# Kernel tuning notes

Measured on AMD Instinct MI355X. Metric: run time of the kernel, lower is better.

Reference implementation:

```python
import jax, jax.numpy as jnp
import numpy as np

N = 70
NT = 2485
M_DIM = 2000
SQ2 = float(np.sqrt(2.0))
SQH = float(np.sqrt(0.5))
_r, _c = np.tril_indices(N)
ROWS = jnp.asarray(_r)
COLS = jnp.asarray(_c)


def smat(x):
    # svec^{-1}: lower-tri fill (row-major) then symmetrize with sqrt(2) off-diag scaling
    v = jnp.reshape(x, (-1,))
    L = jnp.zeros((N, N), v.dtype).at[ROWS, COLS].set(v)
    return SQH * (L + L.T) - (SQ2 - 1.0) * L * jnp.eye(N, dtype=v.dtype)


def svec(X):
    Y = SQ2 * X - (SQ2 - 1.0) * X * jnp.eye(N, dtype=X.dtype)
    return Y[ROWS, COLS].reshape(NT, 1)


def skmult(G, K, Amat):
    # vectorized version of the per-column loop: for each column a of Amat,
    # 0.5 * svec(K smat(a) G^T + G smat(a) K^T)
    S = jax.vmap(smat, in_axes=1)(Amat)                      # [L, N, N]
    T = jnp.einsum('ij,ljk,hk->lih', K, S, G) + jnp.einsum('ij,ljk,hk->lih', G, S, K)
    return jax.vmap(svec)(0.5 * T)[:, :, 0].T                # [NT, L]


def Hp_op(U, P, Pinv):
    return 0.5 * (P @ U @ Pinv + Pinv.T @ U.T @ P.T)


def _steplen(d, Rinv, gcur):
    lam0 = jnp.linalg.eigvalsh(Rinv.T @ smat(d) @ Rinv)[0]   # smallest eigenvalue
    s = jnp.where(lam0 < 0, -1.0 / lam0, 20.0)
    return jnp.minimum(0.5, gcur * s)


def setup_inputs() -> dict:
    key = jax.random.key(0)
    ks = jax.random.split(key, 6)
    R1 = jax.random.normal(ks[0], (N, N), jnp.float32)
    X0 = R1 @ R1.T + N * jnp.eye(N, dtype=jnp.float32)
    R2 = jax.random.normal(ks[1], (N, N), jnp.float32)
    Z0 = R2 @ R2.T + N * jnp.eye(N, dtype=jnp.float32)
    x = svec(X0)
    z = svec(Z0)
    A = jax.random.normal(ks[2], (M_DIM, NT), jnp.float32) / np.float32(np.sqrt(NT))
    y = jax.random.normal(ks[3], (M_DIM, 1), jnp.float32)
    b = A @ x + 0.1 * jax.random.normal(ks[4], (M_DIM, 1), jnp.float32)
    c = z + A.T @ y + 0.1 * jax.random.normal(ks[5], (NT, 1), jnp.float32)
    normc = jnp.full((1, 1), 3.7, jnp.float32)
    return {'x': x, 'y': y, 'z': z, 'A': A, 'b': b, 'c': c, 'normc': normc}


def reference(x, y, z, A, b, c, normc):
    tol = 1e-6
    X = smat(x)
    Z = smat(z)
    Q = jnp.linalg.cholesky(X).T        # upper factor: X = Q^T Q
    P = jnp.linalg.cholesky(Z).T
    Qinv = jnp.linalg.inv(Q)
    Pinv = jnp.linalg.inv(P)
    Zinv = jnp.linalg.inv(Z)
    rp = b - A @ x
    Rd = c - z - A.T @ y
    mu = (x[:, 0] @ z[:, 0]) / 70.0
    # predictor
    Rc = -svec(Hp_op(X @ Z, P, Pinv))
    Mmat = A @ skmult(X, Zinv, A.T)
    Minv = jnp.linalg.inv(Mmat)
    h = rp + A @ (skmult(X, Zinv, Rd) - skmult(Pinv, Pinv, Rc))
    dy = Minv @ h
    dz = Rd - A.T @ dy
    dx = -x - skmult(X, Zinv, dz)
    alpha = _steplen(dx, Qinv, 0.9)
    beta = _steplen(dz, Pinv, 0.9)
    minab = jnp.minimum(alpha, beta)
    e = jnp.where((mu > tol) & (minab >= jnp.sqrt(1.0 / 3.0)),
                  jnp.maximum(1.0, 3.0 * minab * minab), 1.0)
    dot_new = (x + alpha * dx)[:, 0] @ (z + beta * dz)[:, 0]
    frac = dot_new / (x[:, 0] @ z[:, 0])
    frac_safe = jnp.where(dot_new < 0, 1.0, frac)
    sigma = jnp.where(dot_new < 0, 0.8, jnp.minimum(1.0, frac_safe ** e))
    # corrector
    Rc2 = svec(sigma * mu * jnp.eye(N, dtype=x.dtype)
               - Hp_op(X @ Z, P, Pinv)
               - Hp_op(smat(dx) @ smat(dz), P, Pinv))
    h2 = rp + A @ (skmult(X, Zinv, Rd) - skmult(Pinv, Pinv, Rc2))
    dy2 = Minv @ h2
    dz2 = Rd - A.T @ dy2
    dx2 = skmult(Pinv, Pinv, Rc2) - skmult(X, Zinv, dz2)
    g2 = 0.9 + 0.09 * minab
    alpha2 = _steplen(dx2, Qinv, g2)
    beta2 = _steplen(dz2, Pinv, g2)
    x_new = x + alpha2 * dx2
    y_new = y + beta2 * dy2
    z_new = z + beta2 * dz2
    y1 = y_new * normc
    return (x_new, y_new, z_new, y1)
```

## Files before the change

kernel.cpp:

```cpp
#include <hip/hip_runtime.h>
#include <math.h>

#define SQHf 0.70710678118654752440f

struct Pairs16 { int4 q[16]; };

__device__ __forceinline__ void d_t2ij(int t, int& i, int& j) {
    float f = sqrtf(8.0f * (float)t + 1.0f);
    int r = (int)((f - 1.0f) * 0.5f);
    while (((r + 1) * (r + 2)) / 2 <= t) ++r;
    while ((r * (r + 1)) / 2 > t) --r;
    i = r;
    j = t - (r * (r + 1)) / 2;
}

__global__ void k_smat2(const float* __restrict__ v1, float* __restrict__ M1,
                        const float* __restrict__ v2, float* __restrict__ M2) {
    int idx = blockIdx.x * 256 + threadIdx.x;
    if (idx >= 9800) return;
    int which = idx / 4900;
    int e = idx - which * 4900;
    const float* v = which ? v2 : v1;
    float* M = which ? M2 : M1;
    int i = e / 70, j = e % 70;
    int hi = i > j ? i : j, lo = i > j ? j : i;
    float val = v[(hi * (hi + 1)) / 2 + lo];
    M[e] = (i == j) ? val : val * SQHf;
}

__global__ __launch_bounds__(256) void k_chol2(const float* __restrict__ A0, float* __restrict__ R0,
                                               const float* __restrict__ A1, float* __restrict__ R1) {
    const float* A = blockIdx.x ? A1 : A0;
    float* R = blockIdx.x ? R1 : R0;
    __shared__ float S[70][71];
    for (int e = threadIdx.x; e < 4900; e += 256) S[e / 70][e % 70] = A[e];
    __syncthreads();
    for (int k = 0; k < 70; ++k) {
        if (threadIdx.x == 0) S[k][k] = sqrtf(S[k][k]);
        __syncthreads();
        float d = S[k][k];
        for (int i = k + 1 + threadIdx.x; i < 70; i += 256) S[i][k] /= d;
        __syncthreads();
        for (int e = threadIdx.x; e < 4900; e += 256) {
            int i = e / 70, j = e % 70;
            if (j > k && i >= j) S[i][j] -= S[i][k] * S[j][k];
        }
        __syncthreads();
    }
    for (int e = threadIdx.x; e < 4900; e += 256) {
        int i = e / 70, j = e % 70;
        R[e] = (i <= j) ? S[j][i] : 0.0f;
    }
}

__global__ __launch_bounds__(256) void k_trinv2(const float* __restrict__ R0, float* __restrict__ O0,
                                                const float* __restrict__ R1, float* __restrict__ O1) {
    const float* R = blockIdx.x ? R1 : R0;
    float* O = blockIdx.x ? O1 : O0;
    __shared__ float S[70][71];
    __shared__ float V[70][71];
    for (int e = threadIdx.x; e < 4900; e += 256) S[e / 70][e % 70] = R[e];
    __syncthreads();
    int j = threadIdx.x;
    if (j < 70) {
        for (int i = j; i >= 0; --i) {
            float s = (i == j) ? 1.0f : 0.0f;
            for (int k = i + 1; k <= j; ++k) s -= S[i][k] * V[j][k];
            V[j][i] = s / S[i][i];
        }
    }
    __syncthreads();
    for (int e = threadIdx.x; e < 4900; e += 256) {
        int i = e / 70, jj = e % 70;
        O[e] = (i <= jj) ? V[jj][i] : 0.0f;
    }
}

__global__ __launch_bounds__(256) void k_mm70(const float* __restrict__ A, int tA,
                                              const float* __restrict__ B, int tB,
                                              float* __restrict__ C) {
    __shared__ float As[70][71], Bs[70][71];
    for (int e = threadIdx.x; e < 4900; e += 256) {
        int i = e / 70, j = e % 70;
        As[i][j] = tA ? A[j * 70 + i] : A[e];
        Bs[i][j] = tB ? B[j * 70 + i] : B[e];
    }
    __syncthreads();
    for (int e = threadIdx.x; e < 4900; e += 256) {
        int i = e / 70, j = e % 70;
        float s = 0.0f;
        for (int k = 0; k < 70; ++k) s += As[i][k] * Bs[k][j];
        C[e] = s;
    }
}

__global__ __launch_bounds__(256) void k_gemv_rowA(const float* __restrict__ A, long lda, int Kdim,
                                                   const float* __restrict__ v, const float* __restrict__ add,
                                                   float sgn, float* __restrict__ out) {
    int row = blockIdx.x;
    const float* Ar = A + (long)row * lda;
    float s = 0.0f;
    for (int k = threadIdx.x; k < Kdim; k += 256) s += Ar[k] * v[k];
    __shared__ float red[256];
    red[threadIdx.x] = s;
    __syncthreads();
    for (int o = 128; o; o >>= 1) {
        if (threadIdx.x < o) red[threadIdx.x] += red[threadIdx.x + o];
        __syncthreads();
    }
    if (threadIdx.x == 0) out[row] = (add ? add[row] : 0.0f) + sgn * red[0];
}

__global__ __launch_bounds__(256) void k_colAT_part(const float* __restrict__ A, long lda, int M, int Ncols,
                                                    const float* __restrict__ w, float* __restrict__ partial) {
    int j = blockIdx.x * 256 + threadIdx.x;
    int s = blockIdx.y;
    int rpb = (M + gridDim.y - 1) / gridDim.y;
    int i0 = s * rpb, i1 = i0 + rpb < M ? i0 + rpb : M;
    float acc = 0.0f;
    if (j < Ncols)
        for (int i = i0; i < i1; ++i) acc += A[(long)i * lda + j] * w[i];
    if (j < Ncols) partial[(long)s * Ncols + j] = acc;
}
__global__ __launch_bounds__(256) void k_colAT_fin(const float* __restrict__ partial, int S, int Ncols,
                                                   const float* __restrict__ add1, const float* __restrict__ add2,
                                                   float sgn, float* __restrict__ out) {
    int j = blockIdx.x * 256 + threadIdx.x;
    if (j >= Ncols) return;
    float s = 0.0f;
    for (int k = 0; k < S; ++k) s += partial[(long)k * Ncols + j];
    float base = (add1 ? add1[j] : 0.0f) - (add2 ? add2[j] : 0.0f);
    out[j] = base + sgn * s;
}

__global__ __launch_bounds__(256) void k_dots_init(const float* __restrict__ x, const float* __restrict__ z,
                                                   float* __restrict__ sc) {
    __shared__ float red[256];
    float s = 0.0f;
    for (int i = threadIdx.x; i < 2485; i += 256) s += x[i] * z[i];
    red[threadIdx.x] = s;
    __syncthreads();
    for (int o = 128; o; o >>= 1) {
        if (threadIdx.x < o) red[threadIdx.x] += red[threadIdx.x + o];
        __syncthreads();
    }
    if (threadIdx.x == 0) { sc[1] = red[0]; sc[0] = red[0] / 70.0f; }
}
__global__ __launch_bounds__(256) void k_dot_new(const float* __restrict__ x, const float* __restrict__ dx,
                                                 const float* __restrict__ z, const float* __restrict__ dz,
                                                 float* __restrict__ sc) {
    __shared__ float red[256];
    float a = sc[2], b = sc[3];
    float s = 0.0f;
    for (int i = threadIdx.x; i < 2485; i += 256)
        s += (x[i] + a * dx[i]) * (z[i] + b * dz[i]);
    red[threadIdx.x] = s;
    __syncthreads();
    for (int o = 128; o; o >>= 1) {
        if (threadIdx.x < o) red[threadIdx.x] += red[threadIdx.x + o];
        __syncthreads();
    }
    if (threadIdx.x == 0) sc[7] = red[0];
}

__global__ __launch_bounds__(256) void k_rc_chain(const float* __restrict__ X, const float* __restrict__ Z,
                                                  const float* __restrict__ Pu, const float* __restrict__ Pi,
                                                  float* __restrict__ W1out, float* __restrict__ Rc) {
    __shared__ float A[70][71], B[70][71], C[70][71];
    int tid = threadIdx.x;
    for (int e = tid; e < 4900; e += 256) { A[e / 70][e % 70] = X[e]; B[e / 70][e % 70] = Z[e]; }
    __syncthreads();
    for (int e = tid; e < 4900; e += 256) {
        int i = e / 70, j = e % 70;
        float s = 0.0f;
        for (int k = 0; k < 70; ++k) s += A[i][k] * B[k][j];
        C[i][j] = s;
    }
    __syncthreads();
    for (int e = tid; e < 4900; e += 256) A[e / 70][e % 70] = Pu[e];
    __syncthreads();
    for (int e = tid; e < 4900; e += 256) {
        int i = e / 70, j = e % 70;
        float s = 0.0f;
        for (int k = 0; k < 70; ++k) s += A[i][k] * C[k][j];
        B[i][j] = s;
    }
    __syncthreads();
    for (int e = tid; e < 4900; e += 256) A[e / 70][e % 70] = Pi[e];
    __syncthreads();
    for (int e = tid; e < 4900; e += 256) {
        int i = e / 70, j = e % 70;
        float s = 0.0f;
        for (int k = 0; k < 70; ++k) s += B[i][k] * A[k][j];
        C[i][j] = s;
        W1out[e] = s;
    }
    __syncthreads();
    for (int t = tid; t < 2485; t += 256) {
        int i, j;
        d_t2ij(t, i, j);
        float v = (i == j) ? C[i][i] : (C[i][j] + C[j][i]) * SQHf;
        Rc[t] = -v;
    }
}

__global__ __launch_bounds__(256) void k_rc2_chain(const float* __restrict__ dxv, const float* __restrict__ dzv,
                                                   const float* __restrict__ Pu, const float* __restrict__ Pi,
                                                   const float* __restrict__ W1, const float* __restrict__ sc,
                                                   float* __restrict__ Rc2) {
    __shared__ float A[70][71], B[70][71], C[70][71];
    int tid = threadIdx.x;
    for (int e = tid; e < 4900; e += 256) {
        int i = e / 70, j = e % 70;
        int hi = i > j ? i : j, lo = i > j ? j : i;
        float vx = dxv[(hi * (hi + 1)) / 2 + lo];
        float vz = dzv[(hi * (hi + 1)) / 2 + lo];
        A[i][j] = (i == j) ? vx : vx * SQHf;
        B[i][j] = (i == j) ? vz : vz * SQHf;
    }
    __syncthreads();
    for (int e = tid; e < 4900; e += 256) {
        int i = e / 70, j = e % 70;
        float s = 0.0f;
        for (int k = 0; k < 70; ++k) s += A[i][k] * B[k][j];
        C[i][j] = s;
    }
    __syncthreads();
    for (int e = tid; e < 4900; e += 256) A[e / 70][e % 70] = Pu[e];
    __syncthreads();
    for (int e = tid; e < 4900; e += 256) {
        int i = e / 70, j = e % 70;
        float s = 0.0f;
        for (int k = 0; k < 70; ++k) s += A[i][k] * C[k][j];
        B[i][j] = s;
    }
    __syncthreads();
    for (int e = tid; e < 4900; e += 256) A[e / 70][e % 70] = Pi[e];
    __syncthreads();
    for (int e = tid; e < 4900; e += 256) {
        int i = e / 70, j = e % 70;
        float s = 0.0f;
        for (int k = 0; k < 70; ++k) s += B[i][k] * A[k][j];
        C[i][j] = s;
    }
    __syncthreads();
    float sm = sc[13];
    for (int t = tid; t < 2485; t += 256) {
        int i, j;
        d_t2ij(t, i, j);
        if (i == j)
            Rc2[t] = sm - W1[i * 70 + i] - C[i][i];
        else
            Rc2[t] = -(W1[i * 70 + j] + W1[j * 70 + i] + C[i][j] + C[j][i]) * SQHf;
    }
}

__device__ void skmult_body(const float* __restrict__ K, const float* __restrict__ G,
                            const float* __restrict__ a, float* __restrict__ out) {
    __shared__ float S[70][71];
    __shared__ float T1[70][71];
    for (int e = threadIdx.x; e < 4900; e += 256) {
        int i = e / 70, j = e % 70;
        int hi = i > j ? i : j, lo = i > j ? j : i;
        float v = a[(hi * (hi + 1)) / 2 + lo];
        S[i][j] = (i == j) ? v : v * SQHf;
    }
    __syncthreads();
    for (int e = threadIdx.x; e < 4900; e += 256) {
        int i = e / 70, j = e % 70;
        const float* Gr = G + j * 70;
        float s = 0.0f;
        for (int k = 0; k < 70; ++k) s += S[i][k] * Gr[k];
        T1[i][j] = s;
    }
    __syncthreads();
    for (int t = threadIdx.x; t < 2485; t += 256) {
        int i, j;
        d_t2ij(t, i, j);
        const float* Ki = K + i * 70;
        const float* Kj = K + j * 70;
        float wij = 0.0f, wji = 0.0f;
        for (int k = 0; k < 70; ++k) {
            wij += Ki[k] * T1[k][j];
            wji += Kj[k] * T1[k][i];
        }
        out[t] = (i == j) ? wij : (wij + wji) * SQHf;
    }
}
__global__ __launch_bounds__(256) void k_skmult(const float* __restrict__ K, const float* __restrict__ G,
                                                const float* __restrict__ Arows, long ldA,
                                                float* __restrict__ outT, long ldOut) {
    int l = blockIdx.x;
    skmult_body(K, G, Arows + (long)l * ldA, outT + (long)l * ldOut);
}
__global__ __launch_bounds__(256) void k_skmult_pair(const float* __restrict__ K0, const float* __restrict__ G0,
                                                     const float* __restrict__ a0, float* __restrict__ o0,
                                                     const float* __restrict__ K1, const float* __restrict__ G1,
                                                     const float* __restrict__ a1, float* __restrict__ o1) {
    if (blockIdx.x == 0) skmult_body(K0, G0, a0, o0);
    else skmult_body(K1, G1, a1, o1);
}

#define BBM 128
#define BBK 32
__global__ __launch_bounds__(256) void k_gemm_nt_big(const float* __restrict__ A, long lda,
                                                     const float* __restrict__ B, long ldb,
                                                     float* __restrict__ C, long ldc,
                                                     int M, int N, int Kd,
                                                     float alpha, float beta, int lower_only) {
    int row0 = blockIdx.y * BBM, col0 = blockIdx.x * BBM;
    if (row0 >= M || col0 >= N) return;
    if (lower_only && col0 > row0 + BBM - 1) return;
    __shared__ float As[BBK][BBM + 4];
    __shared__ float Bs[BBK][BBM + 4];
    int tid = threadIdx.x;
    int tx = tid & 15, ty = tid >> 4;
    float acc[8][8];
#pragma unroll
    for (int m = 0; m < 8; ++m)
#pragma unroll
        for (int n = 0; n < 8; ++n) acc[m][n] = 0.0f;
    for (int k0 = 0; k0 < Kd; k0 += BBK) {
        for (int e = tid; e < BBM * BBK; e += 256) {
            int r = e >> 5, cc = e & 31;
            int gr = row0 + r, gc = k0 + cc;
            As[cc][r] = (gr < M && gc < Kd) ? A[(long)gr * lda + gc] : 0.0f;
        }
        for (int e = tid; e < BBM * BBK; e += 256) {
            int r = e >> 5, cc = e & 31;
            int gr = col0 + r, gc = k0 + cc;
            Bs[cc][r] = (gr < N && gc < Kd) ? B[(long)gr * ldb + gc] : 0.0f;
        }
        __syncthreads();
        for (int kk = 0; kk < BBK; ++kk) {
            float4 a0 = *(const float4*)&As[kk][ty * 8];
            float4 a1 = *(const float4*)&As[kk][ty * 8 + 4];
            float4 b0 = *(const float4*)&Bs[kk][tx * 8];
            float4 b1 = *(const float4*)&Bs[kk][tx * 8 + 4];
            float av[8] = {a0.x, a0.y, a0.z, a0.w, a1.x, a1.y, a1.z, a1.w};
            float bv[8] = {b0.x, b0.y, b0.z, b0.w, b1.x, b1.y, b1.z, b1.w};
#pragma unroll
            for (int m = 0; m < 8; ++m)
#pragma unroll
                for (int n = 0; n < 8; ++n) acc[m][n] += av[m] * bv[n];
        }
        __syncthreads();
    }
#pragma unroll
    for (int m = 0; m < 8; ++m) {
        int gr = row0 + ty * 8 + m;
        if (gr < M) {
#pragma unroll
            for (int n = 0; n < 8; ++n) {
                int gc = col0 + tx * 8 + n;
                if (gc < N) {
                    float* cp = &C[(long)gr * ldc + gc];
                    if (beta != 0.0f) *cp = beta * (*cp) + alpha * acc[m][n];
                    else *cp = alpha * acc[m][n];
                }
            }
        }
    }
}

__device__ __forceinline__ void gemm_nn_dev(const float* __restrict__ A, long lda,
                                            const float* __restrict__ B, long ldb,
                                            float* __restrict__ C, long ldc,
                                            int M, int N, int K, float alpha) {
    int row0 = blockIdx.y * 64, col0 = blockIdx.x * 64;
    if (row0 >= M || col0 >= N) return;
    __shared__ float As[64][33], Bs[32][65];
    int tid = threadIdx.x;
    int tx = tid % 16, ty = tid / 16;
    float acc[4][4] = {{0.f}};
    for (int k0 = 0; k0 < K; k0 += 32) {
        for (int e = tid; e < 64 * 32; e += 256) {
            int r = e / 32, cc = e % 32;
            As[r][cc] = (row0 + r < M && k0 + cc < K) ? A[(long)(row0 + r) * lda + k0 + cc] : 0.0f;
        }
        for (int e = tid; e < 32 * 64; e += 256) {
            int kk = e / 64, nn = e % 64;
            Bs[kk][nn] = (k0 + kk < K && col0 + nn < N) ? B[(long)(k0 + kk) * ldb + col0 + nn] : 0.0f;
        }
        __syncthreads();
        for (int kk = 0; kk < 32; ++kk) {
            float av[4], bv[4];
#pragma unroll
            for (int m = 0; m < 4; ++m) av[m] = As[ty * 4 + m][kk];
#pragma unroll
            for (int n = 0; n < 4; ++n) bv[n] = Bs[kk][tx * 4 + n];
#pragma unroll
            for (int m = 0; m < 4; ++m)
#pragma unroll
                for (int n = 0; n < 4; ++n) acc[m][n] += av[m] * bv[n];
        }
        __syncthreads();
    }
#pragma unroll
    for (int m = 0; m < 4; ++m)
#pragma unroll
        for (int n = 0; n < 4; ++n) {
            int gr = row0 + ty * 4 + m, gc = col0 + tx * 4 + n;
            if (gr < M && gc < N) C[(long)gr * ldc + gc] = alpha * acc[m][n];
        }
}

__global__ __launch_bounds__(256) void k_tri_phaseA(const float* __restrict__ Mm, long ld,
                                                    float* __restrict__ tmp, Pairs16 pl, int np) {
    int z = blockIdx.z;
    if (z >= np) return;
    int p0 = pl.q[z].x, h = pl.q[z].y, n = pl.q[z].z, toff = pl.q[z].w;
    gemm_nn_dev(Mm + (long)(p0 + h) * ld + p0, ld,
                Mm + (long)p0 * ld + p0, ld,
                tmp + toff, h, n - h, h, h, 1.0f);
}
__global__ __launch_bounds__(256) void k_tri_phaseB(float* __restrict__ Mm, long ld,
                                                    const float* __restrict__ tmp, Pairs16 pl, int np) {
    int z = blockIdx.z;
    if (z >= np) return;
    int p0 = pl.q[z].x, h = pl.q[z].y, n = pl.q[z].z, toff = pl.q[z].w;
    int M = n - h;
    gemm_nn_dev(Mm + (long)(p0 + h) * ld + (p0 + h), ld,
                tmp + toff, h,
                Mm + (long)(p0 + h) * ld + p0, ld, M, h, M, -1.0f);
}

__global__ void k_zero_upper(float* __restrict__ Mm, int n) {
    int row0 = blockIdx.y * 64, col0 = blockIdx.x * 64;
    if (col0 <= row0) return;
    for (int e = threadIdx.x; e < 4096; e += 256) {
        int i = row0 + (e >> 6), j = col0 + (e & 63);
        if (i < n && j < n) Mm[(long)i * n + j] = 0.0f;
    }
}

__global__ void k_copy_diaginv(float* __restrict__ Mm, long ld, int n, const float* __restrict__ Linv) {
    int t = blockIdx.x;
    int jb = t * 64;
    int nb = n - jb < 64 ? n - jb : 64;
    if (nb <= 0) return;
    const float* Vi = Linv + (long)t * 4096;
    for (int e = threadIdx.x; e < nb * nb; e += 256) {
        int i = e / nb, j = e % nb;
        Mm[(long)(jb + i) * ld + jb + j] = Vi[i * 64 + j];
    }
}

__global__ __launch_bounds__(256) void k_trimv_low(const float* __restrict__ W, long ld, int n,
                                                   const float* __restrict__ h, float* __restrict__ out) {
    int i = blockIdx.x;
    const float* Wr = W + (long)i * ld;
    float s = 0.0f;
    for (int k = threadIdx.x; k <= i; k += 256) s += Wr[k] * h[k];
    __shared__ float red[256];
    red[threadIdx.x] = s;
    __syncthreads();
    for (int o = 128; o; o >>= 1) {
        if (threadIdx.x < o) red[threadIdx.x] += red[threadIdx.x + o];
        __syncthreads();
    }
    if (threadIdx.x == 0) out[i] = red[0];
}

__global__ __launch_bounds__(256) void k_trimvT_part(const float* __restrict__ W, long ld, int n,
                                                     const float* __restrict__ v, float* __restrict__ partial) {
    int j = blockIdx.x * 256 + threadIdx.x;
    int s = blockIdx.y;
    int rpb = (n + gridDim.y - 1) / gridDim.y;
    int i0 = s * rpb, i1 = i0 + rpb < n ? i0 + rpb : n;
    float acc = 0.0f;
    if (j < n) {
        int ist = i0 > j ? i0 : j;
        for (int i = ist; i < i1; ++i) acc += W[(long)i * ld + j] * v[i];
        partial[(long)s * n + j] = acc;
    }
}
__global__ __launch_bounds__(256) void k_part_reduce(const float* __restrict__ partial, int S, int n,
                                                     float* __restrict__ out) {
    int j = blockIdx.x * 256 + threadIdx.x;
    if (j >= n) return;
    float s = 0.0f;
    for (int k = 0; k < S; ++k) s += partial[(long)k * n + j];
    out[j] = s;
}

__global__ __launch_bounds__(256) void k_chol_step(float* __restrict__ Mm, long ld, int n,
                                                   int jb, int nb, int rows, int gb, int gb2,
                                                   float* __restrict__ Linv, int* __restrict__ flg) {
    __shared__ float shbuf[8448];
    int tid = threadIdx.x;
    int bid = blockIdx.x;
    int r0 = jb + nb;

    if (bid == 0) {
        float (*S)[65] = (float(*)[65])shbuf;
        float (*V)[65] = (float(*)[65])(shbuf + 4160);
        float* dv = shbuf + 8320;
        for (int e = tid; e < nb * nb; e += 256) S[e / nb][e % nb] = Mm[(long)(jb + e / nb) * ld + jb + e % nb];
        __syncthreads();
        for (int k = 0; k < nb; ++k) {
            float dinv = 1.0f / S[k][k];
            for (int e = tid; e < nb * nb; e += 256) {
                int i = e / nb, j = e % nb;
                if (j > k && i >= j) S[i][j] -= S[i][k] * S[j][k] * dinv;
            }
            __syncthreads();
        }
        if (tid < nb) dv[tid] = rsqrtf(S[tid][tid]);
        __syncthreads();
        for (int e = tid; e < nb * nb; e += 256) {
            int i = e / nb, j = e % nb;
            if (i >= j) S[i][j] *= dv[j];
        }
        __syncthreads();
        for (int e = tid; e < nb * nb; e += 256) {
            int i = e / nb, j = e % nb;
            if (i >= j) Mm[(long)(jb + i) * ld + jb + j] = S[i][j];
        }
        if (tid < nb) {
            int c = tid;
            V[c][c] = 1.0f / S[c][c];
            for (int i = c + 1; i < nb; ++i) {
                float s = 0.0f;
                for (int k = c; k < i; ++k) s += S[i][k] * V[k][c];
                V[i][c] = -s / S[i][i];
            }
        }
        __syncthreads();
        for (int e = tid; e < 4096; e += 256) {
            int i = e >> 6, j = e & 63;
            Linv[e] = (i < nb && j < nb && i >= j) ? V[i][j] : 0.0f;
        }
        __threadfence();
        __syncthreads();
        if (tid == 0) atomicAdd(&flg[0], 1);
    } else if (bid <= gb) {
        float (*Vs)[65] = (float(*)[65])shbuf;
        float (*As)[65] = (float(*)[65])(shbuf + 4160);
        int pr0 = r0 + (bid - 1) * 64;
        int nrows = n - pr0;
        if (nrows > 64) nrows = 64;
        for (int e = tid; e < nrows * nb; e += 256) {
            int i = e / nb, j = e % nb;
            As[i][j] = Mm[(long)(pr0 + i) * ld + jb + j];
        }
        if (tid == 0) {
            while (atomicAdd(&flg[0], 0) == 0) __builtin_amdgcn_s_sleep(2);
        }
        __syncthreads();
        __threadfence();
        for (int e = tid; e < 4096; e += 256) { int i = e >> 6, j = e & 63; Vs[i][j] = Linv[e]; }
        __syncthreads();
        int tx = tid % 16, ty = tid / 16;
        float acc[4][4] = {{0.f}};
        for (int k = 0; k < nb; ++k) {
            float av[4], bv[4];
#pragma unroll
            for (int m = 0; m < 4; ++m) av[m] = As[ty * 4 + m][k];
#pragma unroll
            for (int c = 0; c < 4; ++c) bv[c] = Vs[tx * 4 + c][k];
#pragma unroll
            for (int m = 0; m < 4; ++m)
#pragma unroll
                for (int c = 0; c < 4; ++c) acc[m][c] += av[m] * bv[c];
        }
#pragma unroll
        for (int m = 0; m < 4; ++m)
#pragma unroll
            for (int c = 0; c < 4; ++c) {
                int gr = ty * 4 + m, gc = tx * 4 + c;
                if (gr < nrows && gc < nb) Mm[(long)(pr0 + gr) * ld + jb + gc] = acc[m][c];
            }
        __threadfence();
        __syncthreads();
        if (tid == 0) atomicAdd(&flg[1], 1);
    } else {
        int t = bid - 1 - gb;
        int I, J;
        d_t2ij(t, I, J);
        int row0 = r0 + I * 128, col0 = r0 + J * 128;
        int Mr = rows - I * 128; if (Mr > 128) Mr = 128;
        int Nr = rows - J * 128; if (Nr > 128) Nr = 128;
        if (Mr <= 0 || Nr <= 0) return;
        float (*As)[132] = (float(*)[132])shbuf;
        float (*Bs)[132] = (float(*)[132])(shbuf + 4224);
        if (tid == 0) {
            while (atomicAdd(&flg[1], 0) < gb) __builtin_amdgcn_s_sleep(2);
        }
        __syncthreads();
        __threadfence();
        int tx = tid & 15, ty = tid >> 4;
        float acc[8][8];
#pragma unroll
        for (int m = 0; m < 8; ++m)
#pragma unroll
            for (int nn = 0; nn < 8; ++nn) acc[m][nn] = 0.0f;
        for (int k0 = 0; k0 < nb; k0 += 32) {
            for (int e = tid; e < 128 * 32; e += 256) {
                int r = e >> 5, cc = e & 31;
                int gc = k0 + cc;
                As[cc][r] = (r < Mr && gc < nb) ? Mm[(long)(row0 + r) * ld + jb + gc] : 0.0f;
            }
            for (int e = tid; e < 128 * 32; e += 256) {
                int r = e >> 5, cc = e & 31;
                int gc = k0 + cc;
                Bs[cc][r] = (r < Nr && gc < nb) ? Mm[(long)(col0 + r) * ld + jb + gc] : 0.0f;
            }
            __syncthreads();
            for (int kk = 0; kk < 32; ++kk) {
                float4 a0 = *(const float4*)&As[kk][ty * 8];
                float4 a1 = *(const float4*)&As[kk][ty * 8 + 4];
                float4 b0 = *(const float4*)&Bs[kk][tx * 8];
                float4 b1 = *(const float4*)&Bs[kk][tx * 8 + 4];
                float av[8] = {a0.x, a0.y, a0.z, a0.w, a1.x, a1.y, a1.z, a1.w};
                float bv[8] = {b0.x, b0.y, b0.z, b0.w, b1.x, b1.y, b1.z, b1.w};
#pragma unroll
                for (int m = 0; m < 8; ++m)
#pragma unroll
                    for (int nn = 0; nn < 8; ++nn) acc[m][nn] += av[m] * bv[nn];
            }
            __syncthreads();
        }
#pragma unroll
        for (int m = 0; m < 8; ++m) {
            int gr = ty * 8 + m;
            if (gr < Mr) {
#pragma unroll
                for (int nn = 0; nn < 8; ++nn) {
                    int gc = tx * 8 + nn;
                    if (gc < Nr) {
                        float* cp = &Mm[(long)(row0 + gr) * ld + col0 + gc];
                        *cp = *cp - acc[m][nn];
                    }
                }
            }
        }
    }
}

__device__ __forceinline__ int jac_f(int i, int r) {
    return (i == 0) ? 0 : 1 + ((i - 1 + r) % 69);
}
__global__ __launch_bounds__(256) void k_steplen_eig(const float* __restrict__ dxv, const float* __restrict__ dzv,
                                                     const float* __restrict__ Qi, const float* __restrict__ Pi,
                                                     float* __restrict__ sc, int o0, int o1) {
    const float* v = blockIdx.x ? dzv : dxv;
    const float* Rm = blockIdx.x ? Pi : Qi;
    int outi = blockIdx.x ? o1 : o0;
    __shared__ float S[70][71], T[70][71], A[70][71];
    __shared__ float cs[35], sn[35];
    int tid = threadIdx.x;
    for (int e = tid; e < 4900; e += 256) {
        int i = e / 70, j = e % 70;
        int hi = i > j ? i : j, lo = i > j ? j : i;
        float val = v[(hi * (hi + 1)) / 2 + lo];
        S[i][j] = (i == j) ? val : val * SQHf;
        A[i][j] = Rm[e];
    }
    __syncthreads();
    for (int e = tid; e < 4900; e += 256) {
        int i = e / 70, j = e % 70;
        float s = 0.0f;
        for (int k = 0; k < 70; ++k) s += A[k][i] * S[k][j];
        T[i][j] = s;
    }
    __syncthreads();
    for (int e = tid; e < 4900; e += 256) {
        int i = e / 70, j = e % 70;
        float s = 0.0f;
        for (int k = 0; k < 70; ++k) s += T[i][k] * A[k][j];
        S[i][j] = s;
    }
    __syncthreads();
    for (int sw = 0; sw < 6; ++sw) {
        for (int rr = 0; rr < 69; ++rr) {
            if (tid < 35) {
                int p = jac_f(tid, rr), q = jac_f(69 - tid, rr);
                float app = S[p][p], aqq = S[q][q], apq = S[p][q];
                float cc = 1.0f, ss = 0.0f;
                float denom = fabsf(app) + fabsf(aqq);
                if (fabsf(apq) > 1e-12f * denom + 1e-30f) {
                    float tau = (aqq - app) / (2.0f * apq);
                    float t = ((tau >= 0.0f) ? 1.0f : -1.0f) / (fabsf(tau) + sqrtf(1.0f + tau * tau));
                    cc = 1.0f / sqrtf(1.0f + t * t);
                    ss = t * cc;
                }
                cs[tid] = cc;
                sn[tid] = ss;
            }
            __syncthreads();
            for (int t = tid; t < 1225; t += 256) {
                int a = t / 35, b = t - a * 35;
                int pa = jac_f(a, rr), qa = jac_f(69 - a, rr);
                int pb = jac_f(b, rr), qb = jac_f(69 - b, rr);
                float ca = cs[a], sa = sn[a], cb = cs[b], sb = sn[b];
                float m00 = S[pa][pb], m01 = S[pa][qb], m10 = S[qa][pb], m11 = S[qa][qb];
                float r00 = ca * m00 - sa * m10, r01 = ca * m01 - sa * m11;
                float r10 = sa * m00 + ca * m10, r11 = sa * m01 + ca * m11;
                S[pa][pb] = cb * r00 - sb * r01;
                S[pa][qb] = sb * r00 + cb * r01;
                S[qa][pb] = cb * r10 - sb * r11;
                S[qa][qb] = sb * r10 + cb * r11;
            }
            __syncthreads();
        }
    }
    __shared__ float red[256];
    float mn = 1e30f;
    for (int i = tid; i < 70; i += 256) mn = fminf(mn, S[i][i]);
    red[tid] = mn;
    __syncthreads();
    for (int o = 128; o; o >>= 1) {
        if (tid < o) red[tid] = fminf(red[tid], red[tid + o]);
        __syncthreads();
    }
    if (tid == 0) sc[outi] = red[0];
}

__global__ void k_pred_scalars(float* sc) {
    float l0a = sc[11], l0b = sc[12];
    float sa = (l0a < 0.0f) ? -1.0f / l0a : 20.0f;
    float sb = (l0b < 0.0f) ? -1.0f / l0b : 20.0f;
    float alpha = fminf(0.5f, 0.9f * sa);
    float beta = fminf(0.5f, 0.9f * sb);
    float minab = fminf(alpha, beta);
    sc[2] = alpha;
    sc[3] = beta;
    sc[4] = minab;
    float mu = sc[0];
    sc[5] = (mu > 1e-6f && minab >= 0.57735026918962576f) ? fmaxf(1.0f, 3.0f * minab * minab) : 1.0f;
}
__global__ void k_sigma(float* sc) {
    float dn = sc[7], xz = sc[1], e = sc[5];
    float frac = dn / xz;
    float fs = (dn < 0.0f) ? 1.0f : frac;
    float sig = (dn < 0.0f) ? 0.8f : fminf(1.0f, powf(fs, e));
    sc[6] = sig;
    sc[13] = sig * sc[0];
    sc[8] = 0.9f + 0.09f * sc[4];
}
__global__ void k_corr_scalars(float* sc) {
    float g2 = sc[8];
    float l0a = sc[14], l0b = sc[15];
    float sa = (l0a < 0.0f) ? -1.0f / l0a : 20.0f;
    float sb = (l0b < 0.0f) ? -1.0f / l0b : 20.0f;
    sc[9] = fminf(0.5f, g2 * sa);
    sc[10] = fminf(0.5f, g2 * sb);
}

__global__ void k_axpby(const float* __restrict__ u, const float* __restrict__ v,
                        float a, float b, float* __restrict__ out, int n) {
    int i = blockIdx.x * 256 + threadIdx.x;
    if (i < n) out[i] = a * u[i] + b * v[i];
}

__global__ void k_final(const float* __restrict__ x, const float* __restrict__ y, const float* __restrict__ z,
                        const float* __restrict__ dx2, const float* __restrict__ dy2, const float* __restrict__ dz2,
                        const float* __restrict__ normc, const float* __restrict__ sc, float* __restrict__ out) {
    int i = blockIdx.x * 256 + threadIdx.x;
    float a2 = sc[9], b2 = sc[10];
    if (i < 2485) out[i] = x[i] + a2 * dx2[i];
    else if (i < 4485) { int j = i - 2485; out[i] = y[j] + b2 * dy2[j]; }
    else if (i < 6970) { int j = i - 4485; out[i] = z[j] + b2 * dz2[j]; }
    else if (i < 8970) { int j = i - 6970; out[i] = (y[j] + b2 * dy2[j]) * normc[0]; }
}

extern "C" void kernel_launch(void* const* d_in, const int* in_sizes, int n_in,
                              void* d_out, int out_size, void* d_ws, size_t ws_size,
                              hipStream_t stream) {
    const float* x = (const float*)d_in[0];
    const float* y = (const float*)d_in[1];
    const float* z = (const float*)d_in[2];
    const float* A = (const float*)d_in[3];
    const float* b = (const float*)d_in[4];
    const float* c = (const float*)d_in[5];
    const float* normc = (const float*)d_in[6];
    float* out = (float*)d_out;
    float* ws = (float*)d_ws;

    float* SKT = ws;
    float* Mm = ws + 4970000;
    float* S0 = ws + 8970000;
    float* X = S0;
    float* Z = S0 + 4900;
    float* Qu = S0 + 9800;
    float* Pu = S0 + 14700;
    float* Qi = S0 + 19600;
    float* Pi = S0 + 24500;
    float* Zi = S0 + 29400;
    float* W1 = S0 + 44100;
    float* rp = S0 + 83300;
    float* h = S0 + 85300;
    float* dy = S0 + 87300;
    float* dy2 = S0 + 89300;
    float* h2 = S0 + 91300;
    float* Rd = S0 + 93300;
    float* Rc = S0 + 95785;
    float* k1 = S0 + 98270;
    float* k2 = S0 + 100755;
    float* dz = S0 + 103240;
    float* dx = S0 + 105725;
    float* Rc2 = S0 + 108210;
    float* k2b = S0 + 110695;
    float* dz2 = S0 + 113180;
    float* dx2 = S0 + 115665;
    float* tmpv = S0 + 118150;
    float* sc = S0 + 120635;
    float* Linv = S0 + 121000;
    float* v1 = S0 + 253000;
    float* pbuf = S0 + 256000;
    int* flags = (int*)(S0 + 300000);

    k_smat2<<<39, 256, 0, stream>>>(x, X, z, Z);
    k_chol2<<<2, 256, 0, stream>>>(X, Qu, Z, Pu);
    k_trinv2<<<2, 256, 0, stream>>>(Qu, Qi, Pu, Pi);
    k_mm70<<<1, 256, 0, stream>>>(Pi, 0, Pi, 1, Zi);

    k_gemv_rowA<<<2000, 256, 0, stream>>>(A, 2485L, 2485, x, b, -1.0f, rp);
    k_colAT_part<<<dim3(10, 16), 256, 0, stream>>>(A, 2485L, 2000, 2485, y, pbuf);
    k_colAT_fin<<<10, 256, 0, stream>>>(pbuf, 16, 2485, c, z, -1.0f, Rd);
    k_dots_init<<<1, 256, 0, stream>>>(x, z, sc);

    k_rc_chain<<<1, 256, 0, stream>>>(X, Z, Pu, Pi, W1, Rc);

    k_skmult<<<2000, 256, 0, stream>>>(X, Zi, A, 2485L, SKT, 2485L);
    k_gemm_nt_big<<<dim3(16, 16), 256, 0, stream>>>(A, 2485L, SKT, 2485L, Mm, 2000L,
                                                    2000, 2000, 2485, 1.0f, 0.0f, 1);

    hipMemsetAsync(flags, 0, 32 * 2 * sizeof(int), stream);
    for (int jb = 0; jb < 2000; jb += 64) {
        int nb = (2000 - jb) < 64 ? (2000 - jb) : 64;
        int rows = 2000 - jb - nb;
        int gb = (rows + 63) / 64;
        int gb2 = (rows + 127) / 128;
        int nsyrk = gb2 * (gb2 + 1) / 2;
        int grid = 1 + gb + nsyrk;
        float* Lslot = Linv + (long)(jb / 64) * 4096;
        k_chol_step<<<grid, 256, 0, stream>>>(Mm, 2000L, 2000, jb, nb, rows, gb, gb2,
                                              Lslot, flags + 2 * (jb / 64));
    }

    k_zero_upper<<<dim3(32, 32), 256, 0, stream>>>(Mm, 2000);
    k_copy_diaginv<<<32, 256, 0, stream>>>(Mm, 2000L, 2000, Linv);
    for (int bs = 64; bs < 2000; bs *= 2) {
        Pairs16 pl;
        int np = 0, maxM = 0, toff = 0;
        for (int p0 = 0; p0 + bs < 2000; p0 += 2 * bs) {
            int hh = bs;
            int nn = (2 * bs < 2000 - p0) ? 2 * bs : (2000 - p0);
            pl.q[np].x = p0; pl.q[np].y = hh; pl.q[np].z = nn; pl.q[np].w = toff;
            toff += (nn - hh) * hh;
            if (nn - hh > maxM) maxM = nn - hh;
            ++np;
        }
        if (np == 0) continue;
        dim3 g((bs + 63) / 64, (maxM + 63) / 64, np);
        k_tri_phaseA<<<g, 256, 0, stream>>>(Mm, 2000L, SKT, pl, np);
        k_tri_phaseB<<<g, 256, 0, stream>>>(Mm, 2000L, SKT, pl, np);
    }

    k_skmult_pair<<<2, 256, 0, stream>>>(X, Zi, Rd, k1, Pi, Pi, Rc, k2);
    k_axpby<<<10, 256, 0, stream>>>(k1, k2, 1.0f, -1.0f, tmpv, 2485);
    k_gemv_rowA<<<2000, 256, 0, stream>>>(A, 2485L, 2485, tmpv, rp, 1.0f, h);
    k_trimv_low<<<2000, 256, 0, stream>>>(Mm, 2000L, 2000, h, v1);
    k_trimvT_part<<<dim3(8, 16), 256, 0, stream>>>(Mm, 2000L, 2000, v1, pbuf);
    k_part_reduce<<<8, 256, 0, stream>>>(pbuf, 16, 2000, dy);
    k_colAT_part<<<dim3(10, 16), 256, 0, stream>>>(A, 2485L, 2000, 2485, dy, pbuf);
    k_colAT_fin<<<10, 256, 0, stream>>>(pbuf, 16, 2485, Rd, (const float*)0, -1.0f, dz);
    k_skmult<<<1, 256, 0, stream>>>(X, Zi, dz, 0L, tmpv, 0L);
    k_axpby<<<10, 256, 0, stream>>>(x, tmpv, -1.0f, -1.0f, dx, 2485);

    k_steplen_eig<<<2, 256, 0, stream>>>(dx, dz, Qi, Pi, sc, 11, 12);
    k_pred_scalars<<<1, 1, 0, stream>>>(sc);
    k_dot_new<<<1, 256, 0, stream>>>(x, dx, z, dz, sc);
    k_sigma<<<1, 1, 0, stream>>>(sc);

    k_rc2_chain<<<1, 256, 0, stream>>>(dx, dz, Pu, Pi, W1, sc, Rc2);
    k_skmult<<<1, 256, 0, stream>>>(Pi, Pi, Rc2, 0L, k2b, 0L);
    k_axpby<<<10, 256, 0, stream>>>(k1, k2b, 1.0f, -1.0f, tmpv, 2485);
    k_gemv_rowA<<<2000, 256, 0, stream>>>(A, 2485L, 2485, tmpv, rp, 1.0f, h2);
    k_trimv_low<<<2000, 256, 0, stream>>>(Mm, 2000L, 2000, h2, v1);
    k_trimvT_part<<<dim3(8, 16), 256, 0, stream>>>(Mm, 2000L, 2000, v1, pbuf);
    k_part_reduce<<<8, 256, 0, stream>>>(pbuf, 16, 2000, dy2);
    k_colAT_part<<<dim3(10, 16), 256, 0, stream>>>(A, 2485L, 2000, 2485, dy2, pbuf);
    k_colAT_fin<<<10, 256, 0, stream>>>(pbuf, 16, 2485, Rd, (const float*)0, -1.0f, dz2);
    k_skmult<<<1, 256, 0, stream>>>(X, Zi, dz2, 0L, tmpv, 0L);
    k_axpby<<<10, 256, 0, stream>>>(k2b, tmpv, 1.0f, -1.0f, dx2, 2485);

    k_steplen_eig<<<2, 256, 0, stream>>>(dx2, dz2, Qi, Pi, sc, 14, 15);
    k_corr_scalars<<<1, 1, 0, stream>>>(sc);

    k_final<<<36, 256, 0, stream>>>(x, y, z, dx2, dy2, dz2, normc, sc, out);
}
```

Before: 11.07 ms.

## Split-K the lower-triangular A·SKᵀ product with atomic accumulation; merge prep kernels

The large 2000x2000x2485 lower-triangle GEMM now splits the K dimension four ways over blockIdx.z. Partial results are accumulated with atomicAdd into a zero-initialised output. This raises block count from about 136 to about 544 so the many CUs on the device have work. The two post-Cholesky kernels (zero upper triangle, copy diagonal inverses) are fused into one launch. The cost is an extra memset of the full matrix, atomic traffic, and nondeterministic float summation order.

Result: faster. 10.76 ms (-2.8%).

```diff
diff --git a/kernel.cpp b/kernel.cpp
--- a/kernel.cpp
+++ b/kernel.cpp
@@ -303,14 +303,16 @@
 
 #define BBM 128
 #define BBK 32
-__global__ __launch_bounds__(256) void k_gemm_nt_big(const float* __restrict__ A, long lda,
-                                                     const float* __restrict__ B, long ldb,
-                                                     float* __restrict__ C, long ldc,
-                                                     int M, int N, int Kd,
-                                                     float alpha, float beta, int lower_only) {
+__global__ __launch_bounds__(256) void k_gemm_syrk_splitk(const float* __restrict__ A, long lda,
+                                                          const float* __restrict__ B, long ldb,
+                                                          float* __restrict__ C, long ldc,
+                                                          int M, int N, int Kd, int nz) {
     int row0 = blockIdx.y * BBM, col0 = blockIdx.x * BBM;
     if (row0 >= M || col0 >= N) return;
-    if (lower_only && col0 > row0 + BBM - 1) return;
+    if (col0 > row0 + BBM - 1) return;
+    int kc = (Kd + nz - 1) / nz;
+    int kbeg = blockIdx.z * kc;
+    int kend = kbeg + kc < Kd ? kbeg + kc : Kd;
     __shared__ float As[BBK][BBM + 4];
     __shared__ float Bs[BBK][BBM + 4];
     int tid = threadIdx.x;
@@ -320,16 +322,16 @@
     for (int m = 0; m < 8; ++m)
 #pragma unroll
         for (int n = 0; n < 8; ++n) acc[m][n] = 0.0f;
-    for (int k0 = 0; k0 < Kd; k0 += BBK) {
+    for (int k0 = kbeg; k0 < kend; k0 += BBK) {
         for (int e = tid; e < BBM * BBK; e += 256) {
             int r = e >> 5, cc = e & 31;
             int gr = row0 + r, gc = k0 + cc;
-            As[cc][r] = (gr < M && gc < Kd) ? A[(long)gr * lda + gc] : 0.0f;
+            As[cc][r] = (gr < M && gc < kend) ? A[(long)gr * lda + gc] : 0.0f;
         }
         for (int e = tid; e < BBM * BBK; e += 256) {
             int r = e >> 5, cc = e & 31;
             int gr = col0 + r, gc = k0 + cc;
-            Bs[cc][r] = (gr < N && gc < Kd) ? B[(long)gr * ldb + gc] : 0.0f;
+            Bs[cc][r] = (gr < N && gc < kend) ? B[(long)gr * ldb + gc] : 0.0f;
         }
         __syncthreads();
         for (int kk = 0; kk < BBK; ++kk) {
@@ -353,11 +355,7 @@
 #pragma unroll
             for (int n = 0; n < 8; ++n) {
                 int gc = col0 + tx * 8 + n;
-                if (gc < N) {
-                    float* cp = &C[(long)gr * ldc + gc];
-                    if (beta != 0.0f) *cp = beta * (*cp) + alpha * acc[m][n];
-                    else *cp = alpha * acc[m][n];
-                }
+                if (gc < N) atomicAdd(&C[(long)gr * ldc + gc], acc[m][n]);
             }
         }
     }
@@ -425,24 +423,23 @@
                 Mm + (long)(p0 + h) * ld + p0, ld, M, h, M, -1.0f);
 }
 
-__global__ void k_zero_upper(float* __restrict__ Mm, int n) {
-    int row0 = blockIdx.y * 64, col0 = blockIdx.x * 64;
-    if (col0 <= row0) return;
-    for (int e = threadIdx.x; e < 4096; e += 256) {
-        int i = row0 + (e >> 6), j = col0 + (e & 63);
-        if (i < n && j < n) Mm[(long)i * n + j] = 0.0f;
-    }
-}
-
-__global__ void k_copy_diaginv(float* __restrict__ Mm, long ld, int n, const float* __restrict__ Linv) {
-    int t = blockIdx.x;
-    int jb = t * 64;
-    int nb = n - jb < 64 ? n - jb : 64;
-    if (nb <= 0) return;
-    const float* Vi = Linv + (long)t * 4096;
-    for (int e = threadIdx.x; e < nb * nb; e += 256) {
-        int i = e / nb, j = e % nb;
-        Mm[(long)(jb + i) * ld + jb + j] = Vi[i * 64 + j];
+__global__ void k_prep_W(float* __restrict__ Mm, long ld, int n, const float* __restrict__ Linv) {
+    int bi = blockIdx.y, bj = blockIdx.x;
+    int row0 = bi * 64, col0 = bj * 64;
+    if (bj < bi) return;
+    if (bj > bi) {
+        for (int e = threadIdx.x; e < 4096; e += 256) {
+            int i = row0 + (e >> 6), j = col0 + (e & 63);
+            if (i < n && j < n) Mm[(long)i * ld + j] = 0.0f;
+        }
+    } else {
+        int nb = n - row0 < 64 ? n - row0 : 64;
+        if (nb <= 0) return;
+        const float* Vi = Linv + (long)bi * 4096;
+        for (int e = threadIdx.x; e < nb * nb; e += 256) {
+            int i = e / nb, j = e % nb;
+            Mm[(long)(row0 + i) * ld + row0 + j] = Vi[i * 64 + j];
+        }
     }
 }
 
@@ -824,8 +821,9 @@
     k_rc_chain<<<1, 256, 0, stream>>>(X, Z, Pu, Pi, W1, Rc);
 
     k_skmult<<<2000, 256, 0, stream>>>(X, Zi, A, 2485L, SKT, 2485L);
-    k_gemm_nt_big<<<dim3(16, 16), 256, 0, stream>>>(A, 2485L, SKT, 2485L, Mm, 2000L,
-                                                    2000, 2000, 2485, 1.0f, 0.0f, 1);
+    hipMemsetAsync(Mm, 0, 4000000 * sizeof(float), stream);
+    k_gemm_syrk_splitk<<<dim3(16, 16, 4), 256, 0, stream>>>(A, 2485L, SKT, 2485L, Mm, 2000L,
+                                                            2000, 2000, 2485, 4);
 
     hipMemsetAsync(flags, 0, 32 * 2 * sizeof(int), stream);
     for (int jb = 0; jb < 2000; jb += 64) {
@@ -840,8 +838,7 @@
                                               Lslot, flags + 2 * (jb / 64));
     }
 
-    k_zero_upper<<<dim3(32, 32), 256, 0, stream>>>(Mm, 2000);
-    k_copy_diaginv<<<32, 256, 0, stream>>>(Mm, 2000L, 2000, Linv);
+    k_prep_W<<<dim3(32, 32), 256, 0, stream>>>(Mm, 2000L, 2000, Linv);
     for (int bs = 64; bs < 2000; bs *= 2) {
         Pairs16 pl;
         int np = 0, maxM = 0, toff = 0;
```
